# Performance work log

Hardware: AMD Instinct MI355X
Metric: run time of the kernel (lower is better)

Reference implementation:

```python
import jax, jax.numpy as jnp
import numpy as np

IN_FEATURES = 8388608
OUT_FEATURES = 6


def setup_inputs() -> dict:
    key = jax.random.key(0)
    k1, k2 = jax.random.split(key)
    # input: [in_features, 2]
    inp = jax.random.normal(k1, (IN_FEATURES, 2), dtype=jnp.float32)
    # weight: [out_features=6, in_features]; torch init is normal(mean=-1, std=1)
    weight = jax.random.normal(k2, (OUT_FEATURES, IN_FEATURES), dtype=jnp.float32) - 1.0
    return {"input": inp, "weight": weight}


def reference(input, weight):
    # Rows 0:3 of weight contract with input[:, 0]; rows 3:6 with input[:, 1].
    # output[j] = sum_i weight[j, i] * input[i, 0 if j < 3 else 1]
    out_a = weight[0:3] @ input[:, 0]  # [3]
    out_b = weight[3:6] @ input[:, 1]  # [3]
    return jnp.concatenate([out_a, out_b])  # [6]
```

## Files before the change

kernel.cpp:

```cpp
#include <hip/hip_runtime.h>

#define IN_FEATURES 8388608
#define NB 2048
#define TPB 256

__global__ __launch_bounds__(TPB) void motor_partial(const float4* __restrict__ inp4,
                                                     const float4* __restrict__ w4,
                                                     float* __restrict__ ws) {
    const int NG = IN_FEATURES / 4;
    const int stride = NB * TPB;
    int g = blockIdx.x * TPB + threadIdx.x;

    float acc0 = 0.f, acc1 = 0.f, acc2 = 0.f, acc3 = 0.f, acc4 = 0.f, acc5 = 0.f;

    for (; g < NG; g += stride) {
        float4 i0 = inp4[2 * g];
        float4 i1 = inp4[2 * g + 1];
        float a0 = i0.x, b0 = i0.y, a1 = i0.z, b1 = i0.w;
        float a2 = i1.x, b2 = i1.y, a3 = i1.z, b3 = i1.w;

        const int rowstride = IN_FEATURES / 4;
        float4 w0 = w4[(size_t)0 * rowstride + g];
        float4 w1 = w4[(size_t)1 * rowstride + g];
        float4 w2 = w4[(size_t)2 * rowstride + g];
        float4 w3 = w4[(size_t)3 * rowstride + g];
        float4 w4v = w4[(size_t)4 * rowstride + g];
        float4 w5 = w4[(size_t)5 * rowstride + g];

        acc0 += w0.x * a0 + w0.y * a1 + w0.z * a2 + w0.w * a3;
        acc1 += w1.x * a0 + w1.y * a1 + w1.z * a2 + w1.w * a3;
        acc2 += w2.x * a0 + w2.y * a1 + w2.z * a2 + w2.w * a3;
        acc3 += w3.x * b0 + w3.y * b1 + w3.z * b2 + w3.w * b3;
        acc4 += w4v.x * b0 + w4v.y * b1 + w4v.z * b2 + w4v.w * b3;
        acc5 += w5.x * b0 + w5.y * b1 + w5.z * b2 + w5.w * b3;
    }

    float acc[6] = {acc0, acc1, acc2, acc3, acc4, acc5};

    #pragma unroll
    for (int j = 0; j < 6; ++j) {
        float v = acc[j];
        #pragma unroll
        for (int off = 32; off > 0; off >>= 1)
            v += __shfl_down(v, off, 64);
        acc[j] = v;
    }

    __shared__ float sm[TPB / 64][6];
    const int lane = threadIdx.x & 63;
    const int wave = threadIdx.x >> 6;
    if (lane == 0) {
        #pragma unroll
        for (int j = 0; j < 6; ++j) sm[wave][j] = acc[j];
    }
    __syncthreads();
    if (threadIdx.x == 0) {
        #pragma unroll
        for (int j = 0; j < 6; ++j)
            ws[blockIdx.x * 6 + j] = sm[0][j] + sm[1][j] + sm[2][j] + sm[3][j];
    }
}

__global__ __launch_bounds__(384) void motor_final(const float* __restrict__ ws,
                                                   float* __restrict__ out) {
    const int j = threadIdx.x >> 6;
    const int lane = threadIdx.x & 63;
    float v = 0.f;
    for (int k = lane; k < NB; k += 64) v += ws[k * 6 + j];
    #pragma unroll
    for (int off = 32; off > 0; off >>= 1)
        v += __shfl_down(v, off, 64);
    if (lane == 0) out[j] = v;
}

extern "C" void kernel_launch(void* const* d_in, const int* in_sizes, int n_in,
                              void* d_out, int out_size, void* d_ws, size_t ws_size,
                              hipStream_t stream) {
    const float4* inp4 = (const float4*)d_in[0];
    const float4* w4   = (const float4*)d_in[1];
    float* ws  = (float*)d_ws;
    float* out = (float*)d_out;

    motor_partial<<<NB, TPB, 0, stream>>>(inp4, w4, ws);
    motor_final<<<1, 384, 0, stream>>>(ws, out);
}
```

Measured before the change: 334.5 us.

## Launch one thread per float4 group with nontemporal loads and column-major partials

```diff
diff --git a/kernel.cpp b/kernel.cpp
--- a/kernel.cpp
+++ b/kernel.cpp
@@ -1,41 +1,36 @@
 #include <hip/hip_runtime.h>
 
 #define IN_FEATURES 8388608
-#define NB 2048
+#define NG (IN_FEATURES / 4)
 #define TPB 256
+#define NB (NG / TPB)
 
-__global__ __launch_bounds__(TPB) void motor_partial(const float4* __restrict__ inp4,
-                                                     const float4* __restrict__ w4,
+typedef float f32x4 __attribute__((ext_vector_type(4)));
+
+__global__ __launch_bounds__(TPB) void motor_partial(const f32x4* __restrict__ inp4,
+                                                     const f32x4* __restrict__ w4,
                                                      float* __restrict__ ws) {
-    const int NG = IN_FEATURES / 4;
-    const int stride = NB * TPB;
-    int g = blockIdx.x * TPB + threadIdx.x;
+    const size_t g = (size_t)blockIdx.x * TPB + threadIdx.x;
 
-    float acc0 = 0.f, acc1 = 0.f, acc2 = 0.f, acc3 = 0.f, acc4 = 0.f, acc5 = 0.f;
+    f32x4 i0  = __builtin_nontemporal_load(inp4 + 2 * g);
+    f32x4 i1  = __builtin_nontemporal_load(inp4 + 2 * g + 1);
+    f32x4 w0  = __builtin_nontemporal_load(w4 + 0 * (size_t)NG + g);
+    f32x4 w1  = __builtin_nontemporal_load(w4 + 1 * (size_t)NG + g);
+    f32x4 w2  = __builtin_nontemporal_load(w4 + 2 * (size_t)NG + g);
+    f32x4 w3  = __builtin_nontemporal_load(w4 + 3 * (size_t)NG + g);
+    f32x4 w4v = __builtin_nontemporal_load(w4 + 4 * (size_t)NG + g);
+    f32x4 w5  = __builtin_nontemporal_load(w4 + 5 * (size_t)NG + g);
 
-    for (; g < NG; g += stride) {
-        float4 i0 = inp4[2 * g];
-        float4 i1 = inp4[2 * g + 1];
-        float a0 = i0.x, b0 = i0.y, a1 = i0.z, b1 = i0.w;
-        float a2 = i1.x, b2 = i1.y, a3 = i1.z, b3 = i1.w;
+    const float a0 = i0.x, b0 = i0.y, a1 = i0.z, b1 = i0.w;
+    const float a2 = i1.x, b2 = i1.y, a3 = i1.z, b3 = i1.w;
 
-        const int rowstride = IN_FEATURES / 4;
-        float4 w0 = w4[(size_t)0 * rowstride + g];
-        float4 w1 = w4[(size_t)1 * rowstride + g];
-        float4 w2 = w4[(size_t)2 * rowstride + g];
-        float4 w3 = w4[(size_t)3 * rowstride + g];
-        float4 w4v = w4[(size_t)4 * rowstride + g];
-        float4 w5 = w4[(size_t)5 * rowstride + g];
-
-        acc0 += w0.x * a0 + w0.y * a1 + w0.z * a2 + w0.w * a3;
-        acc1 += w1.x * a0 + w1.y * a1 + w1.z * a2 + w1.w * a3;
-        acc2 += w2.x * a0 + w2.y * a1 + w2.z * a2 + w2.w * a3;
-        acc3 += w3.x * b0 + w3.y * b1 + w3.z * b2 + w3.w * b3;
-        acc4 += w4v.x * b0 + w4v.y * b1 + w4v.z * b2 + w4v.w * b3;
-        acc5 += w5.x * b0 + w5.y * b1 + w5.z * b2 + w5.w * b3;
-    }
-
-    float acc[6] = {acc0, acc1, acc2, acc3, acc4, acc5};
+    float acc[6];
+    acc[0] = w0.x * a0 + w0.y * a1 + w0.z * a2 + w0.w * a3;
+    acc[1] = w1.x * a0 + w1.y * a1 + w1.z * a2 + w1.w * a3;
+    acc[2] = w2.x * a0 + w2.y * a1 + w2.z * a2 + w2.w * a3;
+    acc[3] = w3.x * b0 + w3.y * b1 + w3.z * b2 + w3.w * b3;
+    acc[4] = w4v.x * b0 + w4v.y * b1 + w4v.z * b2 + w4v.w * b3;
+    acc[5] = w5.x * b0 + w5.y * b1 + w5.z * b2 + w5.w * b3;
 
     #pragma unroll
     for (int j = 0; j < 6; ++j) {
@@ -54,10 +49,9 @@
         for (int j = 0; j < 6; ++j) sm[wave][j] = acc[j];
     }
     __syncthreads();
-    if (threadIdx.x == 0) {
-        #pragma unroll
-        for (int j = 0; j < 6; ++j)
-            ws[blockIdx.x * 6 + j] = sm[0][j] + sm[1][j] + sm[2][j] + sm[3][j];
+    if (threadIdx.x < 6) {
+        const int j = threadIdx.x;
+        ws[(size_t)j * NB + blockIdx.x] = sm[0][j] + sm[1][j] + sm[2][j] + sm[3][j];
     }
 }
 
@@ -65,8 +59,13 @@
                                                    float* __restrict__ out) {
     const int j = threadIdx.x >> 6;
     const int lane = threadIdx.x & 63;
+    const f32x4* p = (const f32x4*)(ws + (size_t)j * NB);
     float v = 0.f;
-    for (int k = lane; k < NB; k += 64) v += ws[k * 6 + j];
+    #pragma unroll
+    for (int k = 0; k < NB / 4 / 64; ++k) {
+        f32x4 t = p[(size_t)k * 64 + lane];
+        v += (t.x + t.y) + (t.z + t.w);
+    }
     #pragma unroll
     for (int off = 32; off > 0; off >>= 1)
         v += __shfl_down(v, off, 64);
@@ -76,8 +75,8 @@
 extern "C" void kernel_launch(void* const* d_in, const int* in_sizes, int n_in,
                               void* d_out, int out_size, void* d_ws, size_t ws_size,
                               hipStream_t stream) {
-    const float4* inp4 = (const float4*)d_in[0];
-    const float4* w4   = (const float4*)d_in[1];
+    const f32x4* inp4 = (const f32x4*)d_in[0];
+    const f32x4* w4   = (const f32x4*)d_in[1];
     float* ws  = (float*)d_ws;
     float* out = (float*)d_out;
 
```

New measurement: 298.6 us. 10.8% less time.
